# Kernel optimization log

Hardware: AMD Instinct MI355X
Metric: run time of the kernel (lower is better)

The kernel has to match this reference:

```python
import jax, jax.numpy as jnp
import numpy as np

B, N, C_IN, C_OUT, K, KS = 8, 2048, 64, 64, 20, 20


def _paiconv(x, feature, kernals, one_padding, mlp_w, mlp_b, conv_w, conv_b,
             mlp_out_w, mlp_out_b, bn_gamma, bn_beta):
    b, c, n = feature.shape
    pts = jnp.transpose(x, (0, 2, 1))                       # [B,N,3]
    sq = jnp.sum(pts * pts, axis=-1)                        # [B,N]
    d2 = sq[:, :, None] + sq[:, None, :] - 2.0 * jnp.einsum('bnd,bmd->bnm', pts, pts)
    _, idx = jax.lax.top_k(-d2, K)                          # [B,N,K] nearest (self first)
    bidx = jnp.arange(b)[:, None, None]
    x_neighs = pts[bidx, idx].reshape(b * n, K, 3)          # [BN,K,3]
    x_repeat = jnp.broadcast_to(x_neighs[:, :1, :], x_neighs.shape)
    x_rel = x_neighs - x_repeat                             # [BN,K,3]
    x_dis = jnp.sqrt(jnp.sum(x_rel * x_rel, axis=-1, keepdims=True) + 1e-12)
    x_feats7 = jnp.concatenate([x_repeat, x_rel, x_dis], axis=-1)  # [BN,K,7]
    # pointwise MLP (Conv1d 7->in_c, kernel 1)
    x_feats = jnp.einsum('nkc,oc->nok', x_feats7, mlp_w) + mlp_b[None, :, None]  # [BN,C,K]
    featsT = jnp.transpose(feature, (0, 2, 1))              # [B,N,C]
    neigh_feats = featsT[bidx, idx].reshape(b * n, K, c)    # [BN,K,C]
    feats = jnp.concatenate([jnp.transpose(neigh_feats, (0, 2, 1)), x_feats], axis=1)  # [BN,2C,K]
    # permutation matrix with threshold + double normalization (topkmax)
    perm = jnp.einsum('nkd,dm->nkm', x_rel, kernals) + one_padding  # [BN,K,KS]
    perm = jnp.where(perm > 0, perm, 0.0)
    perm = perm / (jnp.sum(perm, axis=1, keepdims=True) + 1e-6)
    perm = perm * perm
    perm = perm / (jnp.sum(perm, axis=1, keepdims=True) + 1e-6)
    perm = jnp.where(perm > 0.1, perm, 0.0)
    agg = jnp.einsum('nck,nkm->ncm', feats, perm).reshape(b * n, 2 * c * KS)
    out = (agg @ conv_w.T + conv_b).reshape(b, n, C_OUT)
    out = jnp.transpose(out, (0, 2, 1)) \
        + jnp.einsum('bcn,oc->bon', feature, mlp_out_w) + mlp_out_b[None, :, None]
    # BatchNorm1d (training-mode batch stats, biased variance, eps=1e-5)
    mean = jnp.mean(out, axis=(0, 2), keepdims=True)
    var = jnp.var(out, axis=(0, 2), keepdims=True)
    out = (out - mean) / jnp.sqrt(var + 1e-5)
    return out * bn_gamma[None, :, None] + bn_beta[None, :, None]


def setup_inputs() -> dict:
    key = jax.random.key(0)
    ks = jax.random.split(key, 10)
    one_padding = jnp.zeros((K, KS), jnp.float32).at[0, 0].set(1.0)
    return {
        'x': jax.random.normal(ks[0], (B, 3, N), jnp.float32),
        'feature': jax.random.normal(ks[1], (B, C_IN, N), jnp.float32),
        'kernals': jax.random.normal(ks[2], (3, KS), jnp.float32),
        'one_padding': one_padding,
        'mlp_w': jax.random.normal(ks[3], (C_IN, 7), jnp.float32) * 0.2,
        'mlp_b': jnp.zeros((C_IN,), jnp.float32),
        'conv_w': jax.random.normal(ks[4], (C_OUT, 2 * C_IN * KS), jnp.float32) * 0.02,
        'conv_b': jnp.zeros((C_OUT,), jnp.float32),
        'mlp_out_w': jax.random.normal(ks[5], (C_OUT, C_IN), jnp.float32) * 0.1,
        'mlp_out_b': jnp.zeros((C_OUT,), jnp.float32),
        'bn_gamma': jnp.ones((C_OUT,), jnp.float32),
        'bn_beta': jnp.zeros((C_OUT,), jnp.float32),
    }


def reference(x, feature, kernals, one_padding, mlp_w, mlp_b, conv_w, conv_b,
              mlp_out_w, mlp_out_b, bn_gamma, bn_beta):
    return _paiconv(x, feature, kernals, one_padding, mlp_w, mlp_b, conv_w, conv_b,
                    mlp_out_w, mlp_out_b, bn_gamma, bn_beta)
```

## Files before the change

kernel.cpp:

```cpp
#include <hip/hip_runtime.h>
#include <cstddef>

#define BB   8
#define NN   2048
#define CIN  64
#define COUT 64
#define KK   20
#define KSS  20
#define C2   128
#define PPB  4
#define NC   24
#define KT   80
#define AGG_LD 2576


typedef _Float16 h2t  __attribute__((ext_vector_type(2)));
typedef _Float16 f16x8 __attribute__((ext_vector_type(8)));
typedef float    f32x4 __attribute__((ext_vector_type(4)));

__device__ __forceinline__ unsigned pk2(float a, float b) {
    unsigned short ua = __builtin_bit_cast(unsigned short, (_Float16)a);
    unsigned short ub = __builtin_bit_cast(unsigned short, (_Float16)b);
    return (unsigned)ua | ((unsigned)ub << 16);
}

__device__ __forceinline__ unsigned wave_min_u32(unsigned v) {
    unsigned x = v, t;
    t = (unsigned)__builtin_amdgcn_update_dpp((int)x, (int)x, 0x111, 0xf, 0xf, false);
    x = (t < x) ? t : x;
    t = (unsigned)__builtin_amdgcn_update_dpp((int)x, (int)x, 0x112, 0xf, 0xf, false);
    x = (t < x) ? t : x;
    t = (unsigned)__builtin_amdgcn_update_dpp((int)x, (int)x, 0x114, 0xf, 0xf, false);
    x = (t < x) ? t : x;
    t = (unsigned)__builtin_amdgcn_update_dpp((int)x, (int)x, 0x118, 0xf, 0xf, false);
    x = (t < x) ? t : x;
    t = (unsigned)__builtin_amdgcn_update_dpp((int)x, (int)x, 0x142, 0xf, 0xf, false);
    x = (t < x) ? t : x;
    t = (unsigned)__builtin_amdgcn_update_dpp((int)x, (int)x, 0x143, 0xf, 0xf, false);
    x = (t < x) ? t : x;
    return (unsigned)__builtin_amdgcn_readlane((int)x, 63);
}

__device__ __forceinline__ float d2f(float px, float py, float pz,
                                     float qx, float qy, float qz) {
    float dx = px - qx, dy = py - qy, dz = pz - qz;
    return fmaf(dz, dz, fmaf(dy, dy, dx * dx));
}

__global__ __launch_bounds__(256) void prep_kernel(
    const float* __restrict__ cw, const float* __restrict__ mw,
    uint4* __restrict__ aFrag, float* __restrict__ mowT)
{
    int i = blockIdx.x * 256 + threadIdx.x;
    if (i < 4 * KT * 64) {
        int wv = i / (KT * 64);
        int r  = i - wv * (KT * 64);
        int t  = r >> 6, l = r & 63;
        int o  = (wv << 4) + (l & 15);
        int j  = (t << 5) + ((l >> 4) << 3);
        const float* s = cw + (size_t)o * (C2 * KSS) + j;
        uint4 v;
        v.x = pk2(s[0], s[1]);
        v.y = pk2(s[2], s[3]);
        v.z = pk2(s[4], s[5]);
        v.w = pk2(s[6], s[7]);
        aFrag[i] = v;
    }
    if (i < COUT * CIN) {
        int o = i >> 6, c = i & 63;
        mowT[c * COUT + o] = mw[o * CIN + c];
    }
}

__global__ __launch_bounds__(256) void tr_kernel(
    const float* __restrict__ f, float* __restrict__ ft)
{
    __shared__ float tile[64][65];
    const int bt = blockIdx.x;
    const int b  = bt >> 5;
    const int n0 = (bt & 31) << 6;
    const int tn  = threadIdx.x & 63;
    const int tc0 = threadIdx.x >> 6;
#pragma unroll
    for (int r = 0; r < 16; ++r) {
        int c = (r << 2) + tc0;
        tile[c][tn] = f[((size_t)(b * CIN + c)) * NN + n0 + tn];
    }
    __syncthreads();
#pragma unroll
    for (int r = 0; r < 16; ++r) {
        int n = (r << 2) + tc0;
        ft[((size_t)b * NN + n0 + n) * CIN + tn] = tile[tn][n];
    }
}

__global__ __launch_bounds__(256, 4) void knn_kernel(
    const float* __restrict__ x, int* __restrict__ nid)
{
    __shared__ int cand_s[4][32];

    const int tid  = threadIdx.x;
    const int w    = tid >> 6;
    const int lane = tid & 63;
    const int p    = blockIdx.x * 4 + w;
    const int b    = p >> 11;
    const int n    = p & (NN - 1);

    const float* xb0 = x + (size_t)(b * 3 + 0) * NN;
    const float* xb1 = x + (size_t)(b * 3 + 1) * NN;
    const float* xb2 = x + (size_t)(b * 3 + 2) * NN;

    const unsigned long long SENT = 0xFFFFFFFFFFFFFFFFull;
    const float qx = xb0[n], qy = xb1[n], qz = xb2[n];

    unsigned long long c0 = SENT, c1 = SENT, c2 = SENT, c3 = SENT;
#pragma unroll
    for (int jj = 0; jj < 8; ++jj) {
        const int m0 = jj * 256 + lane * 4;
        const float4 vx = *(const float4*)&xb0[m0];
        const float4 vy = *(const float4*)&xb1[m0];
        const float4 vz = *(const float4*)&xb2[m0];
        const float dd4[4] = { d2f(vx.x, vy.x, vz.x, qx, qy, qz),
                               d2f(vx.y, vy.y, vz.y, qx, qy, qz),
                               d2f(vx.z, vy.z, vz.z, qx, qy, qz),
                               d2f(vx.w, vy.w, vz.w, qx, qy, qz) };
#pragma unroll
        for (int e = 0; e < 4; ++e) {
            unsigned long long pk =
                ((unsigned long long)__float_as_uint(dd4[e]) << 32)
                | (unsigned)(m0 + e);
            if (pk < c0)      { c3 = c2; c2 = c1; c1 = c0; c0 = pk; }
            else if (pk < c1) { c3 = c2; c2 = c1; c1 = pk; }
            else if (pk < c2) { c3 = c2; c2 = pk; }
            else if (pk < c3) { c3 = pk; }
        }
    }

    const unsigned dv0 = (unsigned)(c0 >> 32), dv1 = (unsigned)(c1 >> 32);
    const unsigned dv2 = (unsigned)(c2 >> 32), dv3 = (unsigned)(c3 >> 32);

    unsigned pfx = 0u;
    for (int i = 30; i >= 0; --i) {
        unsigned T = pfx | (1u << i);
        int cnt = (int)(dv0 < T) + (int)(dv1 < T) + (int)(dv2 < T) + (int)(dv3 < T);
        unsigned long long B0 = __ballot(cnt & 1);
        unsigned long long B1 = __ballot(cnt & 2);
        unsigned long long B2 = __ballot(cnt & 4);
        int tot = __popcll(B0) + 2 * __popcll(B1) + 4 * __popcll(B2);
        if (tot < NC) pfx = T;
    }
    const unsigned tau = pfx;

    int cle = (int)(dv0 <= tau) + (int)(dv1 <= tau)
            + (int)(dv2 <= tau) + (int)(dv3 <= tau);
    unsigned long long L0 = __ballot(cle & 1);
    unsigned long long L1 = __ballot(cle & 2);
    unsigned long long L2 = __ballot(cle & 4);
    int tot_le = __popcll(L0) + 2 * __popcll(L1) + 4 * __popcll(L2);
    const bool trigger = (tot_le != NC) || (__ballot(cle == 4) != 0ull);

    int ci_cand = 0x7fffffff;
    if (!trigger) {
        unsigned long long below = (1ull << lane) - 1ull;
        int pre = __popcll(L0 & below) + 2 * __popcll(L1 & below);
        if (cle >= 1) cand_s[w][pre + 0] = (int)(unsigned)c0;
        if (cle >= 2) cand_s[w][pre + 1] = (int)(unsigned)c1;
        if (cle >= 3) cand_s[w][pre + 2] = (int)(unsigned)c2;
        if (lane < NC) ci_cand = cand_s[w][lane];
    } else {
        unsigned killmask = 0u;
        unsigned long long mypk = SENT;
        for (int k = 0; k < NC; ++k) {
            unsigned myd  = (unsigned)(c0 >> 32);
            unsigned dmin = wave_min_u32(myd);
            unsigned idxc = (myd == dmin) ? (unsigned)c0 : 0xFFFFFFFFu;
            unsigned imin = wave_min_u32(idxc);
            unsigned long long bp = ((unsigned long long)dmin << 32) | imin;
            if (lane == k) mypk = bp;
            if (c0 == bp) {
                unsigned mi = (unsigned)(bp & 0xFFFFFFFFull);
                killmask |= 1u << (((mi >> 8) << 2) | (mi & 3));
                c0 = c1; c1 = c2; c2 = c3; c3 = SENT;
                if (c0 == SENT) {
                    for (int jj = 0; jj < 8; ++jj) {
                        const int m0 = jj * 256 + lane * 4;
                        const float4 vx = *(const float4*)&xb0[m0];
                        const float4 vy = *(const float4*)&xb1[m0];
                        const float4 vz = *(const float4*)&xb2[m0];
                        const float dd4[4] = { d2f(vx.x, vy.x, vz.x, qx, qy, qz),
                                               d2f(vx.y, vy.y, vz.y, qx, qy, qz),
                                               d2f(vx.z, vy.z, vz.z, qx, qy, qz),
                                               d2f(vx.w, vy.w, vz.w, qx, qy, qz) };
#pragma unroll
                        for (int e = 0; e < 4; ++e) {
                            if (killmask & (1u << ((jj << 2) | e))) continue;
                            unsigned long long pk =
                                ((unsigned long long)__float_as_uint(dd4[e]) << 32)
                                | (unsigned)(m0 + e);
                            if (pk < c0)      { c3 = c2; c2 = c1; c1 = c0; c0 = pk; }
                            else if (pk < c1) { c3 = c2; c2 = c1; c1 = pk; }
                            else if (pk < c2) { c3 = c2; c2 = pk; }
                            else if (pk < c3) { c3 = pk; }
                        }
                    }
                }
            }
        }
        if (lane < NC) ci_cand = (int)(mypk & 0xFFFFFFFFull);
    }

    double dd = 1e300;
    int ci = 0x7fffffff;
    if (lane < NC) {
        ci = ci_cand;
        double dx = (double)xb0[ci] - (double)qx;
        double dy = (double)xb1[ci] - (double)qy;
        double dz = (double)xb2[ci] - (double)qz;
        dd = dx * dx + dy * dy + dz * dz;
    }
    unsigned long long db = __double_as_longlong(dd);
#pragma unroll
    for (int size = 2; size <= 32; size <<= 1) {
#pragma unroll
        for (int stride = size >> 1; stride > 0; stride >>= 1) {
            unsigned long long odb = __shfl_xor(db, stride);
            int oci = __shfl_xor(ci, stride);
            bool up = ((lane & size) == 0);
            bool takemin = (((lane & stride) == 0) == up);
            bool oless = (odb < db) || (odb == db && oci < ci);
            if (takemin == oless) { db = odb; ci = oci; }
        }
    }
    if (lane < KK) nid[(size_t)p * KK + lane] = ci;
}

__global__ __launch_bounds__(256, 3) void point_kernel(
    const float* __restrict__ x,
    const float* __restrict__ featT,
    const float* __restrict__ kern,
    const float* __restrict__ pad,
    const float* __restrict__ mlp_w,
    const float* __restrict__ mlp_b,
    const uint4* __restrict__ aFrag,
    const float* __restrict__ conv_b,
    const float* __restrict__ mowT,
    const float* __restrict__ mob,
    const int* __restrict__ nid,
    float* __restrict__ out)
{
    __shared__ __align__(16) _Float16 agg_h[PPB][AGG_LD];
    __shared__ __align__(16) float u_s[PPB * KK * KSS];
    __shared__ float xr_s[PPB][KK][3];
    __shared__ float xd_s[PPB][KK];
    __shared__ float xrep_s[PPB][3];
    __shared__ float colden_s[PPB][KSS];
    __shared__ float fcol_s[PPB][CIN];
    __shared__ int   nid_s[PPB][KK];

    float (*perm_s)[KK][KSS] = (float (*)[KK][KSS])u_s;
    float (*red2)[COUT]      = (float (*)[COUT])u_s;

    const int tid  = threadIdx.x;
    const int w    = tid >> 6;
    const int lane = tid & 63;
    const int p    = blockIdx.x * PPB + w;
    const int b    = p >> 11;
    const int n    = p & (NN - 1);

    const float* xb0 = x + (size_t)(b * 3 + 0) * NN;
    const float* xb1 = x + (size_t)(b * 3 + 1) * NN;
    const float* xb2 = x + (size_t)(b * 3 + 2) * NN;

    if (lane < KK) nid_s[w][lane] = nid[(size_t)p * KK + lane];

    fcol_s[w][lane] = featT[((size_t)b * NN + n) * CIN + lane];

    if (lane == 0) {
        int m0 = nid_s[w][0];
        xrep_s[w][0] = xb0[m0]; xrep_s[w][1] = xb1[m0]; xrep_s[w][2] = xb2[m0];
    }
    if (lane < KK) {
        int m = nid_s[w][lane];
        float rx = xb0[m] - xrep_s[w][0];
        float ry = xb1[m] - xrep_s[w][1];
        float rz = xb2[m] - xrep_s[w][2];
        xr_s[w][lane][0] = rx; xr_s[w][lane][1] = ry; xr_s[w][lane][2] = rz;
        xd_s[w][lane] = sqrtf(rx * rx + ry * ry + rz * rz + 1e-12f);
    }

    for (int e = lane; e < KK * KSS; e += 64) {
        int k = e / KSS, m = e % KSS;
        float v = xr_s[w][k][0] * kern[0 * KSS + m]
                + xr_s[w][k][1] * kern[1 * KSS + m]
                + xr_s[w][k][2] * kern[2 * KSS + m]
                + pad[k * KSS + m];
        perm_s[w][k][m] = v > 0.0f ? v : 0.0f;
    }
    if (lane < KSS) {
        float s = 0.0f;
        for (int k = 0; k < KK; ++k) s += perm_s[w][k][lane];
        colden_s[w][lane] = s + 1e-6f;
    }
    for (int e = lane; e < KK * KSS; e += 64) {
        int k = e / KSS, m = e % KSS;
        float v = perm_s[w][k][m] / colden_s[w][m];
        perm_s[w][k][m] = v * v;
    }
    if (lane < KSS) {
        float s = 0.0f;
        for (int k = 0; k < KK; ++k) s += perm_s[w][k][lane];
        colden_s[w][lane] = s + 1e-6f;
    }
    for (int e = lane; e < KK * KSS; e += 64) {
        int k = e / KSS, m = e % KSS;
        float v = perm_s[w][k][m] / colden_s[w][m];
        perm_s[w][k][m] = v > 0.1f ? v : 0.0f;
    }

    float fg[KK], fm[KK];
#pragma unroll
    for (int k = 0; k < KK; ++k)
        fg[k] = featT[((size_t)b * NN + nid_s[w][k]) * CIN + lane];
    {
        float w0 = mlp_w[lane * 7 + 0], w1 = mlp_w[lane * 7 + 1];
        float w2 = mlp_w[lane * 7 + 2], w3 = mlp_w[lane * 7 + 3];
        float w4 = mlp_w[lane * 7 + 4], w5 = mlp_w[lane * 7 + 5];
        float w6 = mlp_w[lane * 7 + 6];
        float bias = mlp_b[lane];
#pragma unroll
        for (int k = 0; k < KK; ++k) {
            fm[k] = xrep_s[w][0] * w0 + xrep_s[w][1] * w1 + xrep_s[w][2] * w2
                  + xr_s[w][k][0] * w3 + xr_s[w][k][1] * w4 + xr_s[w][k][2] * w5
                  + xd_s[w][k] * w6 + bias;
        }
    }

#pragma unroll
    for (int m4 = 0; m4 < KSS / 4; ++m4) {
        float sx = 0.f, sy = 0.f, sz = 0.f, sw = 0.f;
        float tx = 0.f, ty = 0.f, tz = 0.f, tw = 0.f;
#pragma unroll
        for (int k = 0; k < KK; ++k) {
            const float4 pv = *(const float4*)&perm_s[w][k][m4 * 4];
            const float a = fg[k], c = fm[k];
            sx += a * pv.x; sy += a * pv.y; sz += a * pv.z; sw += a * pv.w;
            tx += c * pv.x; ty += c * pv.y; tz += c * pv.z; tw += c * pv.w;
        }
        const int mb = m4 * 4;
        agg_h[w][lane * KSS + mb + 0]         = (_Float16)sx;
        agg_h[w][lane * KSS + mb + 1]         = (_Float16)sy;
        agg_h[w][lane * KSS + mb + 2]         = (_Float16)sz;
        agg_h[w][lane * KSS + mb + 3]         = (_Float16)sw;
        agg_h[w][(CIN + lane) * KSS + mb + 0] = (_Float16)tx;
        agg_h[w][(CIN + lane) * KSS + mb + 1] = (_Float16)ty;
        agg_h[w][(CIN + lane) * KSS + mb + 2] = (_Float16)tz;
        agg_h[w][(CIN + lane) * KSS + mb + 3] = (_Float16)tw;
    }
    __syncthreads();

    {
        f32x4 acc0 = {0.f, 0.f, 0.f, 0.f};
        f32x4 acc1 = {0.f, 0.f, 0.f, 0.f};
        const uint4* ap = aFrag + (size_t)(w * KT) * 64 + lane;
        const _Float16* bp = &agg_h[lane & 3][(lane >> 4) * 8];
#pragma unroll 4
    for (int t = 0; t < KT; t += 2) {
            uint4 av0 = ap[(size_t)t * 64];
            uint4 av1 = ap[(size_t)(t + 1) * 64];
            f16x8 b0 = *(const f16x8*)(bp + t * 32);
            f16x8 b1 = *(const f16x8*)(bp + (t + 1) * 32);
            acc0 = __builtin_amdgcn_mfma_f32_16x16x32_f16(
                       __builtin_bit_cast(f16x8, av0), b0, acc0, 0, 0, 0);
            acc1 = __builtin_amdgcn_mfma_f32_16x16x32_f16(
                       __builtin_bit_cast(f16x8, av1), b1, acc1, 0, 0, 0);
        }
        acc0 += acc1;
        if ((lane & 15) < 4) {
            const int p2 = lane & 15;
            const int ob = (w << 4) + ((lane >> 4) << 2);
            *(f32x4*)&red2[p2][ob] = acc0;
        }
    }
    __syncthreads();

    {
        float acc = conv_b[lane] + red2[w][lane];
        for (int c = 0; c < CIN; ++c)
            acc += fcol_s[w][c] * mowT[c * COUT + lane];
        acc += mob[lane];
        out[(size_t)(b * COUT + lane) * NN + n] = acc;
    }
}

__global__ __launch_bounds__(256) void bn_reduce(
    const float* __restrict__ out, float* __restrict__ part)
{
    const int o = blockIdx.x >> 3;
    const int s = blockIdx.x & 7;
    const float* src = out + (size_t)(s * COUT + o) * NN;
    float a = 0.f, q = 0.f;
    for (int i = threadIdx.x; i < NN; i += 256) {
        float v = src[i];
        a += v; q += v * v;
    }
    __shared__ float s1[256], s2[256];
    s1[threadIdx.x] = a; s2[threadIdx.x] = q;
    __syncthreads();
    for (int st = 128; st > 0; st >>= 1) {
        if (threadIdx.x < st) {
            s1[threadIdx.x] += s1[threadIdx.x + st];
            s2[threadIdx.x] += s2[threadIdx.x + st];
        }
        __syncthreads();
    }
    if (threadIdx.x == 0) {
        part[(o * 8 + s) * 2 + 0] = s1[0];
        part[(o * 8 + s) * 2 + 1] = s2[0];
    }
}

__global__ __launch_bounds__(256) void bn_apply(
    float* __restrict__ out, const float* __restrict__ part,
    const float* __restrict__ gamma, const float* __restrict__ beta)
{
    const int o = blockIdx.x >> 3;
    const int s = blockIdx.x & 7;
    float a = 0.f, q = 0.f;
#pragma unroll
    for (int t = 0; t < 8; ++t) {
        a += part[(o * 8 + t) * 2 + 0];
        q += part[(o * 8 + t) * 2 + 1];
    }
    const float M = (float)(BB * NN);
    const float mean = a / M;
    float var = q / M - mean * mean;
    if (var < 0.f) var = 0.f;
    const float inv = 1.0f / sqrtf(var + 1e-5f);
    const float g = gamma[o] * inv, be = beta[o];
    float* dst = out + (size_t)(s * COUT + o) * NN;
    for (int i = threadIdx.x; i < NN; i += 256) {
        dst[i] = (dst[i] - mean) * g + be;
    }
}

extern "C" void kernel_launch(void* const* d_in, const int* in_sizes, int n_in,
                              void* d_out, int out_size, void* d_ws, size_t ws_size,
                              hipStream_t stream)
{
    const float* x       = (const float*)d_in[0];
    const float* feature = (const float*)d_in[1];
    const float* kern    = (const float*)d_in[2];
    const float* pad     = (const float*)d_in[3];
    const float* mlp_w   = (const float*)d_in[4];
    const float* mlp_b   = (const float*)d_in[5];
    const float* conv_w  = (const float*)d_in[6];
    const float* conv_b  = (const float*)d_in[7];
    const float* mow     = (const float*)d_in[8];
    const float* mob     = (const float*)d_in[9];
    const float* gamma   = (const float*)d_in[10];
    const float* beta    = (const float*)d_in[11];

    char* wsp = (char*)d_ws;
    uint4* aFrag = (uint4*)wsp;
    float* mowT  = (float*)(wsp + 327680);
    float* part  = (float*)(wsp + 327680 + 16384);
    int*   nid   = (int*)(wsp + 327680 + 16384 + 4096);
    float* featT = (float*)(wsp + 327680 + 16384 + 4096 + 1310720);

    float* out = (float*)d_out;

    prep_kernel<<<(4 * KT * 64 + 255) / 256, 256, 0, stream>>>(conv_w, mow, aFrag, mowT);
    tr_kernel<<<BB * (NN / 64), 256, 0, stream>>>(feature, featT);
    knn_kernel<<<BB * NN / 4, 256, 0, stream>>>(x, nid);
    point_kernel<<<BB * NN / PPB, 256, 0, stream>>>(x, featT, kern, pad,
                                                    mlp_w, mlp_b, aFrag, conv_b,
                                                    mowT, mob, nid, out);
    bn_reduce<<<512, 256, 0, stream>>>(out, part);
    bn_apply<<<512, 256, 0, stream>>>(out, part, gamma, beta);
}
```

Baseline: 242.0 us.

## Fuse prep, transpose and kNN into one launch; split top-4 insertion chains

Merges the weight-prep, feature-transpose and kNN kernels into a single front kernel that dispatches on block index, removing two launches and letting the independent stages run concurrently. The kNN scan now keeps two independent top-4 lists, one per pair of candidates, and merges them with a min/max network. This shortens the serial compare-and-shift dependency chain. The cost is higher register pressure (launch bounds drop from 4 to 3 blocks per CU) and a merged kernel carrying the transpose tile's shared memory in every block.

```diff
diff --git a/kernel.cpp b/kernel.cpp
--- a/kernel.cpp
+++ b/kernel.cpp
@@ -12,6 +12,10 @@
 #define NC   24
 #define KT   80
 #define AGG_LD 2576
+
+#define PREP_NB 80
+#define TR_NB   256
+#define KNN_NB  (BB * NN / 4)
 
 
 typedef _Float16 h2t  __attribute__((ext_vector_type(2)));
@@ -47,62 +51,88 @@
     return fmaf(dz, dz, fmaf(dy, dy, dx * dx));
 }
 
-__global__ __launch_bounds__(256) void prep_kernel(
+__device__ __forceinline__ unsigned long long umin64(unsigned long long a,
+                                                     unsigned long long b) {
+    return a < b ? a : b;
+}
+__device__ __forceinline__ unsigned long long umax64(unsigned long long a,
+                                                     unsigned long long b) {
+    return a < b ? b : a;
+}
+
+#define INS4(c0, c1, c2, c3, pk) do { \
+    if (pk < c0)      { c3 = c2; c2 = c1; c1 = c0; c0 = pk; } \
+    else if (pk < c1) { c3 = c2; c2 = c1; c1 = pk; } \
+    else if (pk < c2) { c3 = c2; c2 = pk; } \
+    else if (pk < c3) { c3 = pk; } \
+} while (0)
+
+#define MERGE4(r0, r1, r2, r3, a0, a1, a2, a3, b0, b1, b2, b3) do { \
+    r0 = umin64(a0, b0); \
+    r1 = umin64(umin64(a1, b1), umax64(a0, b0)); \
+    r2 = umin64(umin64(a2, b2), umin64(umax64(a0, b1), umax64(a1, b0))); \
+    r3 = umin64(umin64(a3, b3), \
+         umin64(umax64(a0, b2), umin64(umax64(a1, b1), umax64(a2, b0)))); \
+} while (0)
+
+__global__ __launch_bounds__(256, 3) void front_kernel(
     const float* __restrict__ cw, const float* __restrict__ mw,
-    uint4* __restrict__ aFrag, float* __restrict__ mowT)
-{
-    int i = blockIdx.x * 256 + threadIdx.x;
-    if (i < 4 * KT * 64) {
-        int wv = i / (KT * 64);
-        int r  = i - wv * (KT * 64);
-        int t  = r >> 6, l = r & 63;
-        int o  = (wv << 4) + (l & 15);
-        int j  = (t << 5) + ((l >> 4) << 3);
-        const float* s = cw + (size_t)o * (C2 * KSS) + j;
-        uint4 v;
-        v.x = pk2(s[0], s[1]);
-        v.y = pk2(s[2], s[3]);
-        v.z = pk2(s[4], s[5]);
-        v.w = pk2(s[6], s[7]);
-        aFrag[i] = v;
-    }
-    if (i < COUT * CIN) {
-        int o = i >> 6, c = i & 63;
-        mowT[c * COUT + o] = mw[o * CIN + c];
-    }
-}
-
-__global__ __launch_bounds__(256) void tr_kernel(
-    const float* __restrict__ f, float* __restrict__ ft)
+    uint4* __restrict__ aFrag, float* __restrict__ mowT,
+    const float* __restrict__ f, float* __restrict__ ft,
+    const float* __restrict__ x, int* __restrict__ nid)
 {
     __shared__ float tile[64][65];
-    const int bt = blockIdx.x;
-    const int b  = bt >> 5;
-    const int n0 = (bt & 31) << 6;
-    const int tn  = threadIdx.x & 63;
-    const int tc0 = threadIdx.x >> 6;
-#pragma unroll
-    for (int r = 0; r < 16; ++r) {
-        int c = (r << 2) + tc0;
-        tile[c][tn] = f[((size_t)(b * CIN + c)) * NN + n0 + tn];
-    }
-    __syncthreads();
-#pragma unroll
-    for (int r = 0; r < 16; ++r) {
-        int n = (r << 2) + tc0;
-        ft[((size_t)b * NN + n0 + n) * CIN + tn] = tile[tn][n];
-    }
-}
-
-__global__ __launch_bounds__(256, 4) void knn_kernel(
-    const float* __restrict__ x, int* __restrict__ nid)
-{
     __shared__ int cand_s[4][32];
 
-    const int tid  = threadIdx.x;
+    const int blk = blockIdx.x;
+    const int tid = threadIdx.x;
+
+    if (blk < PREP_NB) {
+        int i = blk * 256 + tid;
+        if (i < 4 * KT * 64) {
+            int wv = i / (KT * 64);
+            int r  = i - wv * (KT * 64);
+            int t  = r >> 6, l = r & 63;
+            int o  = (wv << 4) + (l & 15);
+            int j  = (t << 5) + ((l >> 4) << 3);
+            const float* s = cw + (size_t)o * (C2 * KSS) + j;
+            uint4 v;
+            v.x = pk2(s[0], s[1]);
+            v.y = pk2(s[2], s[3]);
+            v.z = pk2(s[4], s[5]);
+            v.w = pk2(s[6], s[7]);
+            aFrag[i] = v;
+        }
+        if (i < COUT * CIN) {
+            int o = i >> 6, c = i & 63;
+            mowT[c * COUT + o] = mw[o * CIN + c];
+        }
+        return;
+    }
+
+    if (blk < PREP_NB + TR_NB) {
+        const int bt = blk - PREP_NB;
+        const int b  = bt >> 5;
+        const int n0 = (bt & 31) << 6;
+        const int tn  = tid & 63;
+        const int tc0 = tid >> 6;
+#pragma unroll
+        for (int r = 0; r < 16; ++r) {
+            int c = (r << 2) + tc0;
+            tile[c][tn] = f[((size_t)(b * CIN + c)) * NN + n0 + tn];
+        }
+        __syncthreads();
+#pragma unroll
+        for (int r = 0; r < 16; ++r) {
+            int n = (r << 2) + tc0;
+            ft[((size_t)b * NN + n0 + n) * CIN + tn] = tile[tn][n];
+        }
+        return;
+    }
+
     const int w    = tid >> 6;
     const int lane = tid & 63;
-    const int p    = blockIdx.x * 4 + w;
+    const int p    = (blk - PREP_NB - TR_NB) * 4 + w;
     const int b    = p >> 11;
     const int n    = p & (NN - 1);
 
@@ -113,28 +143,33 @@
     const unsigned long long SENT = 0xFFFFFFFFFFFFFFFFull;
     const float qx = xb0[n], qy = xb1[n], qz = xb2[n];
 
-    unsigned long long c0 = SENT, c1 = SENT, c2 = SENT, c3 = SENT;
+    unsigned long long a0 = SENT, a1 = SENT, a2 = SENT, a3 = SENT;
+    unsigned long long e0 = SENT, e1 = SENT, e2 = SENT, e3 = SENT;
 #pragma unroll
     for (int jj = 0; jj < 8; ++jj) {
         const int m0 = jj * 256 + lane * 4;
         const float4 vx = *(const float4*)&xb0[m0];
         const float4 vy = *(const float4*)&xb1[m0];
         const float4 vz = *(const float4*)&xb2[m0];
-        const float dd4[4] = { d2f(vx.x, vy.x, vz.x, qx, qy, qz),
-                               d2f(vx.y, vy.y, vz.y, qx, qy, qz),
-                               d2f(vx.z, vy.z, vz.z, qx, qy, qz),
-                               d2f(vx.w, vy.w, vz.w, qx, qy, qz) };
-#pragma unroll
-        for (int e = 0; e < 4; ++e) {
-            unsigned long long pk =
-                ((unsigned long long)__float_as_uint(dd4[e]) << 32)
-                | (unsigned)(m0 + e);
-            if (pk < c0)      { c3 = c2; c2 = c1; c1 = c0; c0 = pk; }
-            else if (pk < c1) { c3 = c2; c2 = c1; c1 = pk; }
-            else if (pk < c2) { c3 = c2; c2 = pk; }
-            else if (pk < c3) { c3 = pk; }
-        }
-    }
+        const float d0 = d2f(vx.x, vy.x, vz.x, qx, qy, qz);
+        const float d1 = d2f(vx.y, vy.y, vz.y, qx, qy, qz);
+        const float d2 = d2f(vx.z, vy.z, vz.z, qx, qy, qz);
+        const float d3 = d2f(vx.w, vy.w, vz.w, qx, qy, qz);
+        unsigned long long pk0 =
+            ((unsigned long long)__float_as_uint(d0) << 32) | (unsigned)(m0 + 0);
+        unsigned long long pk1 =
+            ((unsigned long long)__float_as_uint(d1) << 32) | (unsigned)(m0 + 1);
+        unsigned long long pk2_ =
+            ((unsigned long long)__float_as_uint(d2) << 32) | (unsigned)(m0 + 2);
+        unsigned long long pk3 =
+            ((unsigned long long)__float_as_uint(d3) << 32) | (unsigned)(m0 + 3);
+        INS4(a0, a1, a2, a3, pk0);
+        INS4(a0, a1, a2, a3, pk1);
+        INS4(e0, e1, e2, e3, pk2_);
+        INS4(e0, e1, e2, e3, pk3);
+    }
+    unsigned long long c0, c1, c2, c3;
+    MERGE4(c0, c1, c2, c3, a0, a1, a2, a3, e0, e1, e2, e3);
 
     const unsigned dv0 = (unsigned)(c0 >> 32), dv1 = (unsigned)(c1 >> 32);
     const unsigned dv2 = (unsigned)(c2 >> 32), dv3 = (unsigned)(c3 >> 32);
@@ -197,10 +232,7 @@
                             unsigned long long pk =
                                 ((unsigned long long)__float_as_uint(dd4[e]) << 32)
                                 | (unsigned)(m0 + e);
-                            if (pk < c0)      { c3 = c2; c2 = c1; c1 = c0; c0 = pk; }
-                            else if (pk < c1) { c3 = c2; c2 = c1; c1 = pk; }
-                            else if (pk < c2) { c3 = c2; c2 = pk; }
-                            else if (pk < c3) { c3 = pk; }
+                            INS4(c0, c1, c2, c3, pk);
                         }
                     }
                 }
@@ -364,7 +396,7 @@
         const uint4* ap = aFrag + (size_t)(w * KT) * 64 + lane;
         const _Float16* bp = &agg_h[lane & 3][(lane >> 4) * 8];
 #pragma unroll 4
-    for (int t = 0; t < KT; t += 2) {
+        for (int t = 0; t < KT; t += 2) {
             uint4 av0 = ap[(size_t)t * 64];
             uint4 av1 = ap[(size_t)(t + 1) * 64];
             f16x8 b0 = *(const f16x8*)(bp + t * 32);
@@ -469,9 +501,8 @@
 
     float* out = (float*)d_out;
 
-    prep_kernel<<<(4 * KT * 64 + 255) / 256, 256, 0, stream>>>(conv_w, mow, aFrag, mowT);
-    tr_kernel<<<BB * (NN / 64), 256, 0, stream>>>(feature, featT);
-    knn_kernel<<<BB * NN / 4, 256, 0, stream>>>(x, nid);
+    front_kernel<<<PREP_NB + TR_NB + KNN_NB, 256, 0, stream>>>(
+        conv_w, mow, aFrag, mowT, feature, featT, x, nid);
     point_kernel<<<BB * NN / PPB, 256, 0, stream>>>(x, featT, kern, pad,
                                                     mlp_w, mlp_b, aFrag, conv_b,
                                                     mowT, mob, nid, out);
```

Measured after the change: 235.9 us, median of 3. 1.03x faster.
